# Optimization experiments

Hardware: AMD Instinct MI355X
Metric: run time of the kernel (lower is better)

## Reference

```python
import jax, jax.numpy as jnp
import numpy as np

B, IMG_ROWS, TSTEPS = 64, 32, 128
HID, CIN = 64, 512  # ncde hidden, ncde input dim = 32 * (IMG_ROWS//2)


def _linear(x, w, b):
    return x @ w.T + b


def _conv(x, w, b, pad):
    y = jax.lax.conv_general_dilated(x, w, (1, 1), [(pad, pad), (pad, pad)],
                                     dimension_numbers=('NCHW', 'OIHW', 'NCHW'))
    return y + b[None, :, None, None]


def _maxpool2(x):
    return jax.lax.reduce_window(x, -jnp.inf, jax.lax.max, (1, 1, 2, 2), (1, 1, 2, 2), 'VALID')


def _natural_cubic_coeffs(x):
    # x: [B, L, C], uniform knots t=0..L-1 (h=1). Natural cubic spline.
    L = x.shape[1]
    n = L - 2
    A = 4.0 * jnp.eye(n, dtype=x.dtype) + jnp.eye(n, k=1, dtype=x.dtype) + jnp.eye(n, k=-1, dtype=x.dtype)
    rhs = 6.0 * (x[:, 2:] - 2.0 * x[:, 1:-1] + x[:, :-2])  # [B, n, C]
    Mi = jnp.linalg.solve(A, rhs.transpose(1, 0, 2).reshape(n, -1))
    Mi = Mi.reshape(n, x.shape[0], x.shape[2]).transpose(1, 0, 2)
    M = jnp.pad(Mi, ((0, 0), (1, 1), (0, 0)))  # natural BCs: M0 = M_{L-1} = 0
    a = x[:, :-1]
    b = (x[:, 1:] - x[:, :-1]) - (2.0 * M[:, :-1] + M[:, 1:]) / 6.0
    c = M[:, :-1] / 2.0
    d = (M[:, 1:] - M[:, :-1]) / 6.0
    return a, b, c, d  # each [B, L-1, C]


def _forward(x, conv1_w, conv1_b, conv2_w, conv2_b, att_fc1_w, att_fc1_b,
             att_fc2_w, att_fc2_b, initial_w, initial_b, f1_w, f1_b,
             f2_w, f2_b, out_w, out_b):
    h = jax.nn.relu(_conv(x, conv1_w, conv1_b, pad=2))
    h = jax.nn.relu(_conv(h, conv2_w, conv2_b, pad=1))
    h = _maxpool2(h)  # [B,32,16,T/2]  (dropout is identity in eval)
    att = h.mean(axis=(2, 3))  # AdaptiveAvgPool2d(1)
    att = jax.nn.sigmoid(_linear(jax.nn.relu(_linear(att, att_fc1_w, att_fc1_b)), att_fc2_w, att_fc2_b))
    h = h * att[:, :, None, None]
    h = jnp.transpose(h, (0, 3, 1, 2))
    seq = h.reshape(h.shape[0], h.shape[1], -1)  # [B, L, 512]
    L = seq.shape[1]
    _, sb, sc, sd = _natural_cubic_coeffs(seq)

    z0 = _linear(seq[:, 0], initial_w, initial_b)  # spline.evaluate(t0) == seq[:,0]

    def cdefunc(z):
        u = jax.nn.relu(_linear(z, f1_w, f1_b))
        u = jnp.tanh(_linear(u, f2_w, f2_b))
        return u.reshape(z.shape[0], HID, CIN)

    def dXdt(t):
        seg = jnp.clip(jnp.floor(t).astype(jnp.int32), 0, L - 2)
        fr = t - seg.astype(t.dtype)
        return sb[:, seg] + 2.0 * sc[:, seg] * fr + 3.0 * sd[:, seg] * fr * fr

    def vf(t, z):
        return jnp.einsum('bhc,bc->bh', cdefunc(z), dXdt(t))

    dt = jnp.float32(0.5)
    nsteps = 2 * (L - 1)

    @jax.checkpoint
    def step(z, t):
        k1 = vf(t, z)
        k2 = vf(t + dt / 2, z + dt / 2 * k1)
        k3 = vf(t + dt / 2, z + dt / 2 * k2)
        k4 = vf(t + dt, z + dt * k3)
        return z + dt / 6.0 * (k1 + 2 * k2 + 2 * k3 + k4), None

    ts = jnp.arange(nsteps, dtype=jnp.float32) * dt
    zT, _ = jax.lax.scan(step, z0, ts)
    return _linear(zT, out_w, out_b)


def setup_inputs() -> dict:
    key = jax.random.key(0)
    ks = jax.random.split(key, 10)
    s = lambda k, shape, sc=0.05: (jax.random.normal(k, shape, jnp.float32) * sc)
    z = lambda n: jnp.zeros((n,), jnp.float32)
    return {
        'x': jax.random.normal(ks[0], (B, 1, IMG_ROWS, TSTEPS), jnp.float32),
        'conv1_w': s(ks[1], (32, 1, 5, 5)), 'conv1_b': z(32),
        'conv2_w': s(ks[2], (32, 32, 3, 3)), 'conv2_b': z(32),
        'att_fc1_w': s(ks[3], (4, 32)), 'att_fc1_b': z(4),
        'att_fc2_w': s(ks[4], (32, 4)), 'att_fc2_b': z(32),
        'initial_w': s(ks[5], (HID, CIN)), 'initial_b': z(HID),
        'f1_w': s(ks[6], (128, HID)), 'f1_b': z(128),
        'f2_w': s(ks[7], (CIN * HID, 128)), 'f2_b': z(CIN * HID),
        'out_w': s(ks[8], (2, HID)), 'out_b': z(2),
    }


def reference(x, conv1_w, conv1_b, conv2_w, conv2_b, att_fc1_w, att_fc1_b,
              att_fc2_w, att_fc2_b, initial_w, initial_b, f1_w, f1_b,
              f2_w, f2_b, out_w, out_b):
    return _forward(x, conv1_w, conv1_b, conv2_w, conv2_b, att_fc1_w, att_fc1_b,
                    att_fc2_w, att_fc2_b, initial_w, initial_b, f1_w, f1_b,
                    f2_w, f2_b, out_w, out_b)
```

## Files before the change

### kernel.cpp

```cpp
#include <hip/hip_runtime.h>
#include <hip/hip_bf16.h>
#include <stdint.h>

#define NSTEP 126
#define NEVAL 504
#define POISON 0xAAAAAAAAu

typedef __bf16 v8bf __attribute__((ext_vector_type(8)));
typedef float  v4f  __attribute__((ext_vector_type(4)));

__device__ __forceinline__ unsigned short f2bf(float x) {
  union { float f; uint32_t u; } v; v.f = x;
  uint32_t u = v.u;
  uint32_t r = (u + 0x7FFFu + ((u >> 16) & 1u)) >> 16;
  return (unsigned short)r;
}
__device__ __forceinline__ float bf2f(unsigned short b) {
  union { uint32_t u; float f; } v; v.u = ((uint32_t)b) << 16;
  return v.f;
}
__device__ __forceinline__ uint32_t cvt_pk_bf16(float lo, float hi) {
  uint32_t r;
  asm("v_cvt_pk_bf16_f32 %0, %1, %2" : "=v"(r) : "v"(lo), "v"(hi));
  return r;
}

__global__ void k_detect(const uint32_t* __restrict__ xw, int* flag) {
  __shared__ int cnt;
  if (threadIdx.x == 0) cnt = 0;
  __syncthreads();
  uint32_t w = xw[threadIdx.x];
  int e = (int)((w >> 7) & 0xFF);
  int good = ((e >= 100) && (e <= 144)) || ((w & 0xFFFFu) == 0u);
  atomicAdd(&cnt, good);
  __syncthreads();
  if (threadIdx.x == 0) *flag = (cnt >= 192) ? 1 : 0;
}

#define NCVT 15
struct CvtArgs {
  const void* src[NCVT];
  int dstoff[NCVT];
  int len[NCVT];
  int kind[NCVT];
  int total;
};
__global__ void k_convert(CvtArgs a, float* __restrict__ ws, const int* __restrict__ flag) {
  int f = *flag;
  for (int i = blockIdx.x*256 + threadIdx.x; i < a.total; i += gridDim.x*256) {
    int t = 0; int rem = i;
    while (rem >= a.len[t]) { rem -= a.len[t]; t++; }
    float v = f ? bf2f(((const unsigned short*)a.src[t])[rem])
                : ((const float*)a.src[t])[rem];
    int d;
    if (a.kind[t] == 1) { int h = rem >> 9, c = rem & 511; d = a.dstoff[t] + c*64 + h; }
    else if (a.kind[t] == 2) {
      int co = rem / 288, r2 = rem % 288;
      int ci = r2 / 9, tt = r2 % 9;
      d = a.dstoff[t] + (co >> 4)*4608 + (ci*16 + (co & 15))*9 + tt;
    }
    else d = a.dstoff[t] + rem;
    ws[d] = v;
  }
}

__global__ void k_wbf16(const void* __restrict__ w2src, const void* __restrict__ w1src,
                        unsigned short* __restrict__ w2bf, unsigned short* __restrict__ w1bf,
                        const int* __restrict__ flag) {
  int f = *flag;
  const long N2 = 4194304, N1 = 8192;
  for (long i = (long)blockIdx.x*256 + threadIdx.x; i < N2 + N1; i += (long)gridDim.x*256) {
    if (i < N2) w2bf[i] = f ? ((const unsigned short*)w2src)[i] : f2bf(((const float*)w2src)[i]);
    else { long j = i - N2; w1bf[j] = f ? ((const unsigned short*)w1src)[j] : f2bf(((const float*)w1src)[j]); }
  }
}

__global__ void k_conv1(const float* __restrict__ xf, const float* __restrict__ w,
                        const float* __restrict__ bias, float* __restrict__ h1) {
  int x = threadIdx.x;
  int y = blockIdx.x;
  int b = blockIdx.y;
  const float* xin = xf + (long)b*4096;
  float in[25];
  #pragma unroll
  for (int ky = 0; ky < 5; ky++) {
    int yy = y + ky - 2;
    #pragma unroll
    for (int kx = 0; kx < 5; kx++) {
      int xx = x + kx - 2;
      in[ky*5+kx] = (yy >= 0 && yy < 32 && xx >= 0 && xx < 128) ? xin[yy*128 + xx] : 0.f;
    }
  }
  for (int co = 0; co < 32; co++) {
    float acc = bias[co];
    #pragma unroll
    for (int t = 0; t < 25; t++) acc += in[t] * w[co*25 + t];
    h1[(((long)b*32 + co)*32 + y)*128 + x] = fmaxf(acc, 0.f);
  }
}

#define LD2 132
__global__ __launch_bounds__(256) void k_conv2(const float* __restrict__ h1, const float* __restrict__ w,
                                               const float* __restrict__ bias, float* __restrict__ h2) {
  __shared__ float s[32][3][LD2];
  int y = blockIdx.x, b = blockIdx.y;
  int tid = threadIdx.x;
  for (int i = tid; i < 32*3*LD2; i += 256) {
    int ci = i / (3*LD2);
    int r  = (i / LD2) % 3;
    int xx = i % LD2;
    int yy = y + r - 1, sx = xx - 1;
    float v = 0.f;
    if (yy >= 0 && yy < 32 && sx >= 0 && sx < 128) v = h1[(((long)b*32+ci)*32+yy)*128+sx];
    s[ci][r][xx] = v;
  }
  __syncthreads();
  int x = tid & 127;
  int half = __builtin_amdgcn_readfirstlane(tid >> 7);
  const float* wb = w + half*4608;
  float acc[16];
  #pragma unroll
  for (int i = 0; i < 16; i++) acc[i] = bias[half*16 + i];
  #pragma unroll 2
  for (int ci = 0; ci < 32; ci++) {
    float xv[9];
    #pragma unroll
    for (int r = 0; r < 3; r++)
      #pragma unroll
      for (int k = 0; k < 3; k++) xv[r*3+k] = s[ci][r][x + k];
    #pragma unroll
    for (int co = 0; co < 16; co++) {
      const float* wr = wb + (ci*16 + co)*9;
      #pragma unroll
      for (int t = 0; t < 9; t++) acc[co] += xv[t] * wr[t];
    }
  }
  #pragma unroll
  for (int co = 0; co < 16; co++)
    h2[(((long)b*32 + half*16 + co)*32 + y)*128 + x] = fmaxf(acc[co], 0.f);
}

__global__ void k_pool(const float* __restrict__ h2, float* __restrict__ pooled, float* __restrict__ attm) {
  int bc = blockIdx.x;
  const float* src = h2 + (long)bc*4096;
  float* dst = pooled + (long)bc*1024;
  float sum = 0.f;
  for (int i = threadIdx.x; i < 1024; i += 256) {
    int py = i >> 6, px = i & 63;
    const float* p = src + py*256 + px*2;
    float m = fmaxf(fmaxf(p[0], p[1]), fmaxf(p[128], p[129]));
    dst[i] = m;
    sum += m;
  }
  __shared__ float red[256];
  red[threadIdx.x] = sum;
  __syncthreads();
  for (int s2 = 128; s2 > 0; s2 >>= 1) {
    if (threadIdx.x < s2) red[threadIdx.x] += red[threadIdx.x + s2];
    __syncthreads();
  }
  if (threadIdx.x == 0) attm[bc] = red[0] * (1.f/1024.f);
}

__global__ void k_att(const float* __restrict__ attm, const float* __restrict__ w1, const float* __restrict__ b1,
                      const float* __restrict__ w2, const float* __restrict__ b2, float* __restrict__ atts) {
  int b = threadIdx.x;
  if (b < 64) {
    float hb[4];
    #pragma unroll
    for (int j = 0; j < 4; j++) {
      float s = b1[j];
      for (int i = 0; i < 32; i++) s += attm[b*32+i]*w1[j*32+i];
      hb[j] = fmaxf(s, 0.f);
    }
    for (int o = 0; o < 32; o++) {
      float s = b2[o];
      #pragma unroll
      for (int j = 0; j < 4; j++) s += hb[j]*w2[o*4+j];
      atts[b*32+o] = 1.f/(1.f + __expf(-s));
    }
  }
}

__global__ void k_seq(const float* __restrict__ pooled, const float* __restrict__ atts, float* __restrict__ seq) {
  for (int idx = blockIdx.x*256 + threadIdx.x; idx < 64*64*512; idx += gridDim.x*256) {
    int b = idx >> 15;
    int t = (idx >> 9) & 63;
    int fch = idx & 511;
    int c = fch >> 4, hh = fch & 15;
    seq[idx] = pooled[(((long)b*32 + c)*16 + hh)*64 + t] * atts[b*32 + c];
  }
}

__global__ __launch_bounds__(256, 1) void k_spline(const float* __restrict__ seq,
                                                   float* __restrict__ dxt) {
  int id = blockIdx.x*256 + threadIdx.x;
  int b = id >> 9, f = id & 511;
  const float* xp = seq + (long)b*32768 + f;
  float xv[64];
  #pragma unroll
  for (int t = 0; t < 64; t++) xv[t] = xp[t*512];
  float cp[62], dp[62];
  float pc = 0.f, pd = 0.f;
  #pragma unroll
  for (int i = 0; i < 62; i++) {
    float rhs = 6.f*(xv[i+2] - 2.f*xv[i+1] + xv[i]);
    float inv = 1.f/(4.f - pc);
    pc = inv;
    pd = (rhs - pd)*inv;
    cp[i] = pc; dp[i] = pd;
  }
  #pragma unroll
  for (int i = 60; i >= 0; i--) dp[i] = dp[i] - cp[i]*dp[i+1];
  const float i6 = 1.f/6.f;
  float* op = dxt + (long)b*512 + f;
  #pragma unroll
  for (int t = 0; t < 63; t++) {
    float M0 = (t == 0)  ? 0.f : dp[t-1];
    float M1 = (t == 62) ? 0.f : dp[t];
    float sb = (xv[t+1] - xv[t]) - (2.f*M0 + M1)*i6;
    float sc = 0.5f*M0;
    float sd = (M1 - M0)*i6;
    float* o = op + (long)(4*t)*32768;
    o[0]      = sb;
    o[32768]  = sb + 0.5f*sc + 0.1875f*sd;
    o[65536]  = sb + sc + 0.75f*sd;
    o[98304]  = sb + 1.5f*sc + 1.6875f*sd;
    if (t == 62) o[131072] = sb + 2.f*sc + 3.f*sd;
  }
}

__global__ void k_z0(const float* __restrict__ seq, const float* __restrict__ iwT,
                     const float* __restrict__ ib, float* __restrict__ z0) {
  __shared__ float s0[512];
  int b = blockIdx.x, h = threadIdx.x;
  for (int c = h; c < 512; c += 64) s0[c] = seq[(long)b*32768 + c];
  __syncthreads();
  float acc = ib[h];
  for (int c = 0; c < 512; c++) acc += s0[c]*iwT[c*64 + h];
  z0[b*64 + h] = acc;
}

__global__ __launch_bounds__(512, 2) void k_ode(
    const float* __restrict__ z0buf,
    const unsigned short* __restrict__ w2bf,
    const unsigned short* __restrict__ w1bf,
    const float* __restrict__ f1bias,
    const float* __restrict__ f2bias,
    const float* __restrict__ dxt,
    const float* __restrict__ outw,
    const float* __restrict__ outb,
    uint32_t* kpart,
    void* dout,
    const int* __restrict__ flag)
{
  __shared__ __align__(16) unsigned short zs[16*72];
  __shared__ __align__(16) unsigned short ub[16*136];
  __shared__ __align__(16) float dxs[16*524 + 9600];
  __shared__ __align__(16) uint32_t klds[1024];
  __shared__ float kred[128];

  int tid = threadIdx.x;
  int bl  = blockIdx.x;
  int hb  = bl >> 2;
  int bq  = bl & 3;
  int B0  = bq*16;
  int lane = tid & 63, wv = tid >> 6;
  int q = lane >> 4, ln = lane & 15;

  v8bf w2f[4][4];
  #pragma unroll
  for (int jt = 0; jt < 4; jt++)
    #pragma unroll
    for (int ks = 0; ks < 4; ks++) {
      long row = (long)hb*512 + wv*64 + jt*16 + ln;
      w2f[jt][ks] = *(const v8bf*)(w2bf + row*128 + ks*32 + q*8);
    }
  v8bf w1f[2];
  #pragma unroll
  for (int ks = 0; ks < 2; ks++)
    w1f[ks] = *(const v8bf*)(w1bf + (wv*16 + ln)*64 + ks*32 + q*8);
  float fb2[4][4];
  #pragma unroll
  for (int jt = 0; jt < 4; jt++)
    #pragma unroll
    for (int r = 0; r < 4; r++)
      fb2[jt][r] = f2bias[(long)hb*512 + wv*64 + jt*16 + q*4 + r];
  float fb1[4];
  #pragma unroll
  for (int r = 0; r < 4; r++)
    fb1[r] = f1bias[wv*16 + q*4 + r];

  int zbL = tid & 15;
  int hg  = tid >> 4;
  int h0  = hg*2;
  float z[2], zacc[2];
  #pragma unroll
  for (int i = 0; i < 2; i++) { z[i] = z0buf[(B0+zbL)*64 + h0 + i]; zacc[i] = 0.f; }

  const float dt6 = 0.5f/6.f;
  int e = 0;
  for (int step = 0; step < NSTEP; step++) {
    #pragma unroll 1
    for (int stage = 0; stage < 4; stage++, e++) {
      bool do_dx = (stage == 1) || (stage == 3) || (e == 0);
      int m = 2*step + ((stage + 1) >> 1);
      float4 dxr[4];
      if (do_dx) {
        #pragma unroll
        for (int i = 0; i < 4; i++) {
          int fi = i*512 + tid;
          int bb = fi >> 7, c4 = fi & 127;
          dxr[i] = *(const float4*)(dxt + (long)m*32768 + (B0+bb)*512 + c4*4);
        }
      }
      if (e > 0) {
        const uint32_t* kp = kpart + ((long)(e-1)*4 + bq)*1024;
        if (tid >= 64 && tid < 320) {
          int pt = tid - 64;
          const uint32_t* pp = kp + pt*4;
          uint32_t v0 = __hip_atomic_load(pp+0, __ATOMIC_RELAXED, __HIP_MEMORY_SCOPE_AGENT);
          uint32_t v1 = __hip_atomic_load(pp+1, __ATOMIC_RELAXED, __HIP_MEMORY_SCOPE_AGENT);
          uint32_t v2 = __hip_atomic_load(pp+2, __ATOMIC_RELAXED, __HIP_MEMORY_SCOPE_AGENT);
          uint32_t v3 = __hip_atomic_load(pp+3, __ATOMIC_RELAXED, __HIP_MEMORY_SCOPE_AGENT);
          while (v0 == POISON) { __builtin_amdgcn_s_sleep(1);
            v0 = __hip_atomic_load(pp+0, __ATOMIC_RELAXED, __HIP_MEMORY_SCOPE_AGENT); }
          while (v1 == POISON) { __builtin_amdgcn_s_sleep(1);
            v1 = __hip_atomic_load(pp+1, __ATOMIC_RELAXED, __HIP_MEMORY_SCOPE_AGENT); }
          while (v2 == POISON) { __builtin_amdgcn_s_sleep(1);
            v2 = __hip_atomic_load(pp+2, __ATOMIC_RELAXED, __HIP_MEMORY_SCOPE_AGENT); }
          while (v3 == POISON) { __builtin_amdgcn_s_sleep(1);
            v3 = __hip_atomic_load(pp+3, __ATOMIC_RELAXED, __HIP_MEMORY_SCOPE_AGENT); }
          uint4 w4; w4.x = v0; w4.y = v1; w4.z = v2; w4.w = v3;
          *(uint4*)(klds + pt*4) = w4;
        }
        __syncthreads();
        if (do_dx) {
          #pragma unroll
          for (int i = 0; i < 4; i++) {
            int fi = i*512 + tid;
            int bb = fi >> 7, c4 = fi & 127;
            *(float4*)(dxs + bb*524 + c4*4) = dxr[i];
          }
        }
        float kv0 = __uint_as_float(klds[h0*16 + zbL]);
        float kv1 = __uint_as_float(klds[(h0+1)*16 + zbL]);
        if (stage == 0) {
          z[0] += dt6*(zacc[0] + kv0);
          z[1] += dt6*(zacc[1] + kv1);
          zacc[0] = 0.f; zacc[1] = 0.f;
          *(uint32_t*)(zs + zbL*72 + h0) = cvt_pk_bf16(z[0], z[1]);
        } else {
          float wk = (stage == 1) ? 1.f : 2.f;
          float aa = (stage == 3) ? 0.5f : 0.25f;
          zacc[0] += wk*kv0;
          zacc[1] += wk*kv1;
          *(uint32_t*)(zs + zbL*72 + h0) = cvt_pk_bf16(z[0] + aa*kv0, z[1] + aa*kv1);
        }
      } else {
        *(uint32_t*)(zs + zbL*72 + h0) = cvt_pk_bf16(z[0], z[1]);
        if (do_dx) {
          #pragma unroll
          for (int i = 0; i < 4; i++) {
            int fi = i*512 + tid;
            int bb = fi >> 7, c4 = fi & 127;
            *(float4*)(dxs + bb*524 + c4*4) = dxr[i];
          }
        }
      }
      __syncthreads();
      v8bf zf[2];
      #pragma unroll
      for (int ks = 0; ks < 2; ks++)
        zf[ks] = *(const v8bf*)(zs + ln*72 + ks*32 + q*8);
      {
        v4f ua = (v4f){fb1[0], fb1[1], fb1[2], fb1[3]};
        #pragma unroll
        for (int ks = 0; ks < 2; ks++)
          ua = __builtin_amdgcn_mfma_f32_16x16x32_bf16(w1f[ks], zf[ks], ua, 0, 0, 0);
        uint2 upk;
        upk.x = cvt_pk_bf16(fmaxf(ua[0], 0.f), fmaxf(ua[1], 0.f));
        upk.y = cvt_pk_bf16(fmaxf(ua[2], 0.f), fmaxf(ua[3], 0.f));
        *(uint2*)(ub + ln*136 + wv*16 + q*4) = upk;
      }
      __syncthreads();
      v8bf uf[4];
      #pragma unroll
      for (int ks = 0; ks < 4; ks++)
        uf[ks] = *(const v8bf*)(ub + ln*136 + ks*32 + q*8);
      float ksum = 0.f;
      #pragma unroll
      for (int jt = 0; jt < 4; jt++) {
        v4f acc = (v4f){fb2[jt][0], fb2[jt][1], fb2[jt][2], fb2[jt][3]};
        #pragma unroll
        for (int ks = 0; ks < 4; ks++)
          acc = __builtin_amdgcn_mfma_f32_16x16x32_bf16(w2f[jt][ks], uf[ks], acc, 0, 0, 0);
        v4f dx4 = *(const v4f*)(dxs + ln*524 + wv*64 + jt*16 + q*4);
        #pragma unroll
        for (int r = 0; r < 4; r++) {
          float xv2 = acc[r];
          float ex = __expf(2.f*xv2);
          float th = 1.f - 2.f*__builtin_amdgcn_rcpf(ex + 1.f);
          ksum += th*dx4[r];
        }
      }
      ksum += __shfl_xor(ksum, 16, 64);
      ksum += __shfl_xor(ksum, 32, 64);
      if (lane < 16)
        kred[ln*8 + wv] = ksum;
      __syncthreads();
      if (tid < 16) {
        const float* kr = kred + tid*8;
        float v = ((((((kr[0]+kr[1])+kr[2])+kr[3])+kr[4])+kr[5])+kr[6])+kr[7];
        uint32_t uv = __float_as_uint(v);
        if (uv == POISON) uv ^= 1u;
        __hip_atomic_store(kpart + (((long)e*4 + bq)*64 + hb)*16 + tid, uv,
                           __ATOMIC_RELAXED, __HIP_MEMORY_SCOPE_AGENT);
      }
    }
  }
  if (hb == 0) {
    const uint32_t* kp = kpart + ((long)(NEVAL-1)*4 + bq)*1024;
    if (tid >= 64 && tid < 128) {
      const uint32_t* pp = kp + (tid - 64)*16;
      while (__hip_atomic_load(pp, __ATOMIC_RELAXED, __HIP_MEMORY_SCOPE_AGENT) == POISON)
        __builtin_amdgcn_s_sleep(1);
    }
    __syncthreads();
    {
      #pragma unroll
      for (int i = 0; i < 2; i++) {
        const uint32_t* p = kp + (h0+i)*16 + zbL;
        uint32_t v = __hip_atomic_load(p, __ATOMIC_RELAXED, __HIP_MEMORY_SCOPE_AGENT);
        while (v == POISON) {
          __builtin_amdgcn_s_sleep(1);
          v = __hip_atomic_load(p, __ATOMIC_RELAXED, __HIP_MEMORY_SCOPE_AGENT);
        }
        z[i] += dt6*(zacc[i] + __uint_as_float(v));
      }
    }
    float o0 = z[0]*outw[h0] + z[1]*outw[h0+1];
    float o1 = z[0]*outw[64+h0] + z[1]*outw[64+h0+1];
    __syncthreads();
    dxs[hg*32 + zbL*2 + 0] = o0;
    dxs[hg*32 + zbL*2 + 1] = o1;
    __syncthreads();
    if (tid < 32) {
      int bloc = tid >> 1, comp = tid & 1;
      float s = outb[comp];
      #pragma unroll
      for (int g = 0; g < 32; g++) s += dxs[g*32 + bloc*2 + comp];
      int b = B0 + bloc;
      if (*flag) ((unsigned short*)dout)[b*2 + comp] = f2bf(s);
      else       ((float*)dout)[b*2 + comp] = s;
    }
  }
}

extern "C" void kernel_launch(void* const* d_in, const int* in_sizes, int n_in,
                              void* d_out, int out_size, void* d_ws, size_t ws_size,
                              hipStream_t stream) {
  (void)in_sizes; (void)n_in; (void)out_size; (void)ws_size;
  float* ws = (float*)d_ws;
  size_t o = 0;
  auto alloc = [&](size_t n) { size_t r = o; o += (n + 63) & ~(size_t)63; return r; };
  size_t o_flag = alloc(64);
  size_t o_xf   = alloc(262144);
  size_t o_c1w  = alloc(800);
  size_t o_c1b  = alloc(32);
  size_t o_c2w  = alloc(9216);
  size_t o_c2b  = alloc(32);
  size_t o_a1w  = alloc(128);
  size_t o_a1b  = alloc(4);
  size_t o_a2w  = alloc(128);
  size_t o_a2b  = alloc(32);
  size_t o_iwT  = alloc(32768);
  size_t o_ib   = alloc(64);
  size_t o_f1b  = alloc(128);
  size_t o_f2b  = alloc(32768);
  size_t o_ow   = alloc(128);
  size_t o_ob   = alloc(2);
  size_t o_z0   = alloc(4096);
  size_t o_attm = alloc(2048);
  size_t o_atts = alloc(2048);
  size_t o_w1bf = alloc(4096);
  size_t o_w2bf = alloc(2097152);
  size_t o_h1   = alloc(8388608);
  size_t o_h2   = alloc(8388608);
  size_t o_kpart= alloc(4128768);
  size_t o_pool = o_h1;
  size_t o_seq  = o_h1 + 2097152;
  size_t o_dxt  = o_h2;

  int* flag = (int*)(ws + o_flag);

  hipLaunchKernelGGL(k_detect, dim3(1), dim3(256), 0, stream, (const uint32_t*)d_in[0], flag);

  CvtArgs ca;
  const int  si[NCVT]  = {0,1,2,3,4,5,6,7,8,9,10,12,14,15,16};
  const size_t dofs[NCVT] = {o_xf,o_c1w,o_c1b,o_c2w,o_c2b,o_a1w,o_a1b,o_a2w,o_a2b,o_iwT,o_ib,o_f1b,o_f2b,o_ow,o_ob};
  const int  ln[NCVT]  = {262144,800,32,9216,32,128,4,128,32,32768,64,128,32768,128,2};
  int tot = 0;
  for (int i = 0; i < NCVT; i++) {
    ca.src[i] = d_in[si[i]];
    ca.dstoff[i] = (int)dofs[i];
    ca.len[i] = ln[i];
    ca.kind[i] = (si[i] == 9) ? 1 : ((si[i] == 3) ? 2 : 0);
    tot += ln[i];
  }
  ca.total = tot;
  hipLaunchKernelGGL(k_convert, dim3(512), dim3(256), 0, stream, ca, ws, flag);
  hipLaunchKernelGGL(k_wbf16, dim3(2048), dim3(256), 0, stream, d_in[13], d_in[11],
                     (unsigned short*)(ws + o_w2bf), (unsigned short*)(ws + o_w1bf), flag);
  hipLaunchKernelGGL(k_conv1, dim3(32,64), dim3(128), 0, stream, ws+o_xf, ws+o_c1w, ws+o_c1b, ws+o_h1);
  hipLaunchKernelGGL(k_conv2, dim3(32,64), dim3(256), 0, stream, ws+o_h1, ws+o_c2w, ws+o_c2b, ws+o_h2);
  hipLaunchKernelGGL(k_pool, dim3(2048), dim3(256), 0, stream, ws+o_h2, ws+o_pool, ws+o_attm);
  hipLaunchKernelGGL(k_att, dim3(1), dim3(64), 0, stream, ws+o_attm, ws+o_a1w, ws+o_a1b, ws+o_a2w, ws+o_a2b, ws+o_atts);
  hipLaunchKernelGGL(k_seq, dim3(2048), dim3(256), 0, stream, ws+o_pool, ws+o_atts, ws+o_seq);
  hipLaunchKernelGGL(k_spline, dim3(128), dim3(256), 0, stream, ws+o_seq, ws+o_dxt);
  hipLaunchKernelGGL(k_z0, dim3(64), dim3(64), 0, stream, ws+o_seq, ws+o_iwT, ws+o_ib, ws+o_z0);

  hipLaunchKernelGGL(k_ode, dim3(256), dim3(512), 0, stream,
                     ws + o_z0,
                     (const unsigned short*)(ws + o_w2bf),
                     (const unsigned short*)(ws + o_w1bf),
                     ws + o_f1b, ws + o_f2b,
                     ws + o_dxt, ws + o_ow, ws + o_ob,
                     (uint32_t*)(ws + o_kpart),
                     d_out, (const int*)flag);
}
```

Measured before the change: 1.704 ms.

## Interleave two batch quarters per ODE block to hide cross-block spin latency

Each ODE block now processes two independent 16-sample batch groups in alternation, with half as many blocks launched. While one group waits for its cross-block k-partial exchange, the other group computes, and the poll of the other group's partials is issued early. The dx spline slice is prefetched into registers one stage ahead, and the barriers become raw s_barrier calls that wait only on LDS counters. This trades per-block parallelism and higher register and LDS use for hiding the serial inter-block dependency latency.

```diff
diff --git a/kernel.cpp b/kernel.cpp
--- a/kernel.cpp
+++ b/kernel.cpp
@@ -24,6 +24,8 @@
   asm("v_cvt_pk_bf16_f32 %0, %1, %2" : "=v"(r) : "v"(lo), "v"(hi));
   return r;
 }
+
+#define BARL() asm volatile("s_waitcnt lgkmcnt(0)\n\ts_barrier" ::: "memory")
 
 __global__ void k_detect(const uint32_t* __restrict__ xw, int* flag) {
   __shared__ int cnt;
@@ -241,6 +243,7 @@
   z0[b*64 + h] = acc;
 }
 
+#define DXSZ (16*524 + 1024)
 __global__ __launch_bounds__(512, 2) void k_ode(
     const float* __restrict__ z0buf,
     const unsigned short* __restrict__ w2bf,
@@ -256,15 +259,16 @@
 {
   __shared__ __align__(16) unsigned short zs[16*72];
   __shared__ __align__(16) unsigned short ub[16*136];
-  __shared__ __align__(16) float dxs[16*524 + 9600];
-  __shared__ __align__(16) uint32_t klds[1024];
+  __shared__ __align__(16) float dxsA[DXSZ];
+  __shared__ __align__(16) float dxsB[DXSZ];
   __shared__ float kred[128];
 
   int tid = threadIdx.x;
   int bl  = blockIdx.x;
-  int hb  = bl >> 2;
-  int bq  = bl & 3;
-  int B0  = bq*16;
+  int hb  = bl >> 1;
+  int bqp = bl & 1;
+  int cqA = bqp,     B0A = bqp*16;
+  int cqB = bqp + 2, B0B = bqp*16 + 32;
   int lane = tid & 63, wv = tid >> 6;
   int q = lane >> 4, ln = lane & 15;
 
@@ -294,140 +298,154 @@
   int zbL = tid & 15;
   int hg  = tid >> 4;
   int h0  = hg*2;
-  float z[2], zacc[2];
-  #pragma unroll
-  for (int i = 0; i < 2; i++) { z[i] = z0buf[(B0+zbL)*64 + h0 + i]; zacc[i] = 0.f; }
+  float zA[2], zaA[2], zB[2], zaB[2];
+  #pragma unroll
+  for (int i = 0; i < 2; i++) {
+    zA[i] = z0buf[(B0A+zbL)*64 + h0 + i]; zaA[i] = 0.f;
+    zB[i] = z0buf[(B0B+zbL)*64 + h0 + i]; zaB[i] = 0.f;
+  }
+
+  uint32_t kvA[2], kvB[2];
+  float4 dxrA[4], dxrB[4];
+  #pragma unroll
+  for (int i = 0; i < 4; i++) {
+    int fi = i*512 + tid;
+    int bb = fi >> 7, c4 = fi & 127;
+    dxrA[i] = *(const float4*)(dxt + (B0A+bb)*512 + c4*4);
+    dxrB[i] = *(const float4*)(dxt + (B0B+bb)*512 + c4*4);
+  }
 
   const float dt6 = 0.5f/6.f;
-  int e = 0;
-  for (int step = 0; step < NSTEP; step++) {
-    #pragma unroll 1
-    for (int stage = 0; stage < 4; stage++, e++) {
-      bool do_dx = (stage == 1) || (stage == 3) || (e == 0);
-      int m = 2*step + ((stage + 1) >> 1);
-      float4 dxr[4];
-      if (do_dx) {
-        #pragma unroll
-        for (int i = 0; i < 4; i++) {
-          int fi = i*512 + tid;
-          int bb = fi >> 7, c4 = fi & 127;
-          dxr[i] = *(const float4*)(dxt + (long)m*32768 + (B0+bb)*512 + c4*4);
+
+  auto STAGE = [&](int e, int cq, int B0,
+                   float (&z)[2], float (&za)[2], uint32_t (&kv)[2],
+                   float4 (&dxr)[4], float (&dxs)[DXSZ],
+                   int eIs, int cqIs, uint32_t (&kvIs)[2], bool isValid) {
+    int st = e & 3;
+    bool dodx = (e & 1) || (e == 0);
+    if (isValid) {
+      const uint32_t* kp2 = kpart + ((long)eIs*4 + cqIs)*1024;
+      kvIs[0] = __hip_atomic_load(kp2 + (h0+0)*16 + zbL, __ATOMIC_RELAXED, __HIP_MEMORY_SCOPE_AGENT);
+      kvIs[1] = __hip_atomic_load(kp2 + (h0+1)*16 + zbL, __ATOMIC_RELAXED, __HIP_MEMORY_SCOPE_AGENT);
+    }
+    if (e > 0) {
+      const uint32_t* kp = kpart + ((long)(e-1)*4 + cq)*1024;
+      float kvf[2];
+      #pragma unroll
+      for (int i = 0; i < 2; i++) {
+        uint32_t v = kv[i];
+        const uint32_t* p = kp + (h0+i)*16 + zbL;
+        while (v == POISON) {
+          __builtin_amdgcn_s_sleep(1);
+          v = __hip_atomic_load(p, __ATOMIC_RELAXED, __HIP_MEMORY_SCOPE_AGENT);
         }
-      }
-      if (e > 0) {
-        const uint32_t* kp = kpart + ((long)(e-1)*4 + bq)*1024;
-        if (tid >= 64 && tid < 320) {
-          int pt = tid - 64;
-          const uint32_t* pp = kp + pt*4;
-          uint32_t v0 = __hip_atomic_load(pp+0, __ATOMIC_RELAXED, __HIP_MEMORY_SCOPE_AGENT);
-          uint32_t v1 = __hip_atomic_load(pp+1, __ATOMIC_RELAXED, __HIP_MEMORY_SCOPE_AGENT);
-          uint32_t v2 = __hip_atomic_load(pp+2, __ATOMIC_RELAXED, __HIP_MEMORY_SCOPE_AGENT);
-          uint32_t v3 = __hip_atomic_load(pp+3, __ATOMIC_RELAXED, __HIP_MEMORY_SCOPE_AGENT);
-          while (v0 == POISON) { __builtin_amdgcn_s_sleep(1);
-            v0 = __hip_atomic_load(pp+0, __ATOMIC_RELAXED, __HIP_MEMORY_SCOPE_AGENT); }
-          while (v1 == POISON) { __builtin_amdgcn_s_sleep(1);
-            v1 = __hip_atomic_load(pp+1, __ATOMIC_RELAXED, __HIP_MEMORY_SCOPE_AGENT); }
-          while (v2 == POISON) { __builtin_amdgcn_s_sleep(1);
-            v2 = __hip_atomic_load(pp+2, __ATOMIC_RELAXED, __HIP_MEMORY_SCOPE_AGENT); }
-          while (v3 == POISON) { __builtin_amdgcn_s_sleep(1);
-            v3 = __hip_atomic_load(pp+3, __ATOMIC_RELAXED, __HIP_MEMORY_SCOPE_AGENT); }
-          uint4 w4; w4.x = v0; w4.y = v1; w4.z = v2; w4.w = v3;
-          *(uint4*)(klds + pt*4) = w4;
+        kvf[i] = __uint_as_float(v);
+      }
+      if (st == 0) {
+        z[0] += dt6*(za[0] + kvf[0]);
+        z[1] += dt6*(za[1] + kvf[1]);
+        za[0] = 0.f; za[1] = 0.f;
+        *(uint32_t*)(zs + zbL*72 + h0) = cvt_pk_bf16(z[0], z[1]);
+      } else {
+        float wk = (st == 1) ? 1.f : 2.f;
+        float aa = (st == 3) ? 0.5f : 0.25f;
+        za[0] += wk*kvf[0];
+        za[1] += wk*kvf[1];
+        *(uint32_t*)(zs + zbL*72 + h0) = cvt_pk_bf16(z[0] + aa*kvf[0], z[1] + aa*kvf[1]);
+      }
+    } else {
+      *(uint32_t*)(zs + zbL*72 + h0) = cvt_pk_bf16(z[0], z[1]);
+    }
+    if (dodx) {
+      #pragma unroll
+      for (int i = 0; i < 4; i++) {
+        int fi = i*512 + tid;
+        int bb = fi >> 7, c4 = fi & 127;
+        *(float4*)(dxs + bb*524 + c4*4) = dxr[i];
+      }
+    }
+    if (!(e & 1)) {
+      int mn = ((e+1) >> 2)*2 + ((((e+1) & 3) + 1) >> 1);
+      #pragma unroll
+      for (int i = 0; i < 4; i++) {
+        int fi = i*512 + tid;
+        int bb = fi >> 7, c4 = fi & 127;
+        dxr[i] = *(const float4*)(dxt + (long)mn*32768 + (B0+bb)*512 + c4*4);
+      }
+    }
+    BARL();
+    v8bf zf[2];
+    #pragma unroll
+    for (int ks = 0; ks < 2; ks++)
+      zf[ks] = *(const v8bf*)(zs + ln*72 + ks*32 + q*8);
+    {
+      v4f ua = (v4f){fb1[0], fb1[1], fb1[2], fb1[3]};
+      #pragma unroll
+      for (int ks = 0; ks < 2; ks++)
+        ua = __builtin_amdgcn_mfma_f32_16x16x32_bf16(w1f[ks], zf[ks], ua, 0, 0, 0);
+      uint2 upk;
+      upk.x = cvt_pk_bf16(fmaxf(ua[0], 0.f), fmaxf(ua[1], 0.f));
+      upk.y = cvt_pk_bf16(fmaxf(ua[2], 0.f), fmaxf(ua[3], 0.f));
+      *(uint2*)(ub + ln*136 + wv*16 + q*4) = upk;
+    }
+    BARL();
+    v8bf uf[4];
+    #pragma unroll
+    for (int ks = 0; ks < 4; ks++)
+      uf[ks] = *(const v8bf*)(ub + ln*136 + ks*32 + q*8);
+    float ksum = 0.f;
+    #pragma unroll
+    for (int jt = 0; jt < 4; jt++) {
+      v4f acc = (v4f){fb2[jt][0], fb2[jt][1], fb2[jt][2], fb2[jt][3]};
+      #pragma unroll
+      for (int ks = 0; ks < 4; ks++)
+        acc = __builtin_amdgcn_mfma_f32_16x16x32_bf16(w2f[jt][ks], uf[ks], acc, 0, 0, 0);
+      v4f dx4 = *(const v4f*)(dxs + ln*524 + wv*64 + jt*16 + q*4);
+      #pragma unroll
+      for (int r = 0; r < 4; r++) {
+        float xv2 = acc[r];
+        float ex = __expf(2.f*xv2);
+        float th = 1.f - 2.f*__builtin_amdgcn_rcpf(ex + 1.f);
+        ksum += th*dx4[r];
+      }
+    }
+    ksum += __shfl_xor(ksum, 16, 64);
+    ksum += __shfl_xor(ksum, 32, 64);
+    if (lane < 16)
+      kred[ln*8 + wv] = ksum;
+    BARL();
+    if (tid < 16) {
+      const float* kr = kred + tid*8;
+      float v = ((((((kr[0]+kr[1])+kr[2])+kr[3])+kr[4])+kr[5])+kr[6])+kr[7];
+      uint32_t uv = __float_as_uint(v);
+      if (uv == POISON) uv ^= 1u;
+      __hip_atomic_store(kpart + (((long)e*4 + cq)*64 + hb)*16 + tid, uv,
+                         __ATOMIC_RELAXED, __HIP_MEMORY_SCOPE_AGENT);
+    }
+  };
+
+  #pragma unroll 1
+  for (int e = 0; e < NEVAL; e++) {
+    STAGE(e, cqA, B0A, zA, zaA, kvA, dxrA, dxsA, e-1, cqB, kvB, (e >= 1));
+    STAGE(e, cqB, B0B, zB, zaB, kvB, dxrB, dxsB, e,   cqA, kvA, true);
+  }
+
+  if (hb == 0) {
+    {
+      const uint32_t* kp = kpart + ((long)(NEVAL-1)*4 + cqA)*1024;
+      #pragma unroll
+      for (int i = 0; i < 2; i++) {
+        uint32_t v = kvA[i];
+        const uint32_t* p = kp + (h0+i)*16 + zbL;
+        while (v == POISON) {
+          __builtin_amdgcn_s_sleep(1);
+          v = __hip_atomic_load(p, __ATOMIC_RELAXED, __HIP_MEMORY_SCOPE_AGENT);
         }
-        __syncthreads();
-        if (do_dx) {
-          #pragma unroll
-          for (int i = 0; i < 4; i++) {
-            int fi = i*512 + tid;
-            int bb = fi >> 7, c4 = fi & 127;
-            *(float4*)(dxs + bb*524 + c4*4) = dxr[i];
-          }
-        }
-        float kv0 = __uint_as_float(klds[h0*16 + zbL]);
-        float kv1 = __uint_as_float(klds[(h0+1)*16 + zbL]);
-        if (stage == 0) {
-          z[0] += dt6*(zacc[0] + kv0);
-          z[1] += dt6*(zacc[1] + kv1);
-          zacc[0] = 0.f; zacc[1] = 0.f;
-          *(uint32_t*)(zs + zbL*72 + h0) = cvt_pk_bf16(z[0], z[1]);
-        } else {
-          float wk = (stage == 1) ? 1.f : 2.f;
-          float aa = (stage == 3) ? 0.5f : 0.25f;
-          zacc[0] += wk*kv0;
-          zacc[1] += wk*kv1;
-          *(uint32_t*)(zs + zbL*72 + h0) = cvt_pk_bf16(z[0] + aa*kv0, z[1] + aa*kv1);
-        }
-      } else {
-        *(uint32_t*)(zs + zbL*72 + h0) = cvt_pk_bf16(z[0], z[1]);
-        if (do_dx) {
-          #pragma unroll
-          for (int i = 0; i < 4; i++) {
-            int fi = i*512 + tid;
-            int bb = fi >> 7, c4 = fi & 127;
-            *(float4*)(dxs + bb*524 + c4*4) = dxr[i];
-          }
-        }
-      }
-      __syncthreads();
-      v8bf zf[2];
-      #pragma unroll
-      for (int ks = 0; ks < 2; ks++)
-        zf[ks] = *(const v8bf*)(zs + ln*72 + ks*32 + q*8);
-      {
-        v4f ua = (v4f){fb1[0], fb1[1], fb1[2], fb1[3]};
-        #pragma unroll
-        for (int ks = 0; ks < 2; ks++)
-          ua = __builtin_amdgcn_mfma_f32_16x16x32_bf16(w1f[ks], zf[ks], ua, 0, 0, 0);
-        uint2 upk;
-        upk.x = cvt_pk_bf16(fmaxf(ua[0], 0.f), fmaxf(ua[1], 0.f));
-        upk.y = cvt_pk_bf16(fmaxf(ua[2], 0.f), fmaxf(ua[3], 0.f));
-        *(uint2*)(ub + ln*136 + wv*16 + q*4) = upk;
-      }
-      __syncthreads();
-      v8bf uf[4];
-      #pragma unroll
-      for (int ks = 0; ks < 4; ks++)
-        uf[ks] = *(const v8bf*)(ub + ln*136 + ks*32 + q*8);
-      float ksum = 0.f;
-      #pragma unroll
-      for (int jt = 0; jt < 4; jt++) {
-        v4f acc = (v4f){fb2[jt][0], fb2[jt][1], fb2[jt][2], fb2[jt][3]};
-        #pragma unroll
-        for (int ks = 0; ks < 4; ks++)
-          acc = __builtin_amdgcn_mfma_f32_16x16x32_bf16(w2f[jt][ks], uf[ks], acc, 0, 0, 0);
-        v4f dx4 = *(const v4f*)(dxs + ln*524 + wv*64 + jt*16 + q*4);
-        #pragma unroll
-        for (int r = 0; r < 4; r++) {
-          float xv2 = acc[r];
-          float ex = __expf(2.f*xv2);
-          float th = 1.f - 2.f*__builtin_amdgcn_rcpf(ex + 1.f);
-          ksum += th*dx4[r];
-        }
-      }
-      ksum += __shfl_xor(ksum, 16, 64);
-      ksum += __shfl_xor(ksum, 32, 64);
-      if (lane < 16)
-        kred[ln*8 + wv] = ksum;
-      __syncthreads();
-      if (tid < 16) {
-        const float* kr = kred + tid*8;
-        float v = ((((((kr[0]+kr[1])+kr[2])+kr[3])+kr[4])+kr[5])+kr[6])+kr[7];
-        uint32_t uv = __float_as_uint(v);
-        if (uv == POISON) uv ^= 1u;
-        __hip_atomic_store(kpart + (((long)e*4 + bq)*64 + hb)*16 + tid, uv,
-                           __ATOMIC_RELAXED, __HIP_MEMORY_SCOPE_AGENT);
-      }
-    }
-  }
-  if (hb == 0) {
-    const uint32_t* kp = kpart + ((long)(NEVAL-1)*4 + bq)*1024;
-    if (tid >= 64 && tid < 128) {
-      const uint32_t* pp = kp + (tid - 64)*16;
-      while (__hip_atomic_load(pp, __ATOMIC_RELAXED, __HIP_MEMORY_SCOPE_AGENT) == POISON)
-        __builtin_amdgcn_s_sleep(1);
-    }
-    __syncthreads();
+        zA[i] += dt6*(zaA[i] + __uint_as_float(v));
+      }
+    }
     {
+      const uint32_t* kp = kpart + ((long)(NEVAL-1)*4 + cqB)*1024;
       #pragma unroll
       for (int i = 0; i < 2; i++) {
         const uint32_t* p = kp + (h0+i)*16 + zbL;
@@ -436,23 +454,43 @@
           __builtin_amdgcn_s_sleep(1);
           v = __hip_atomic_load(p, __ATOMIC_RELAXED, __HIP_MEMORY_SCOPE_AGENT);
         }
-        z[i] += dt6*(zacc[i] + __uint_as_float(v));
-      }
-    }
-    float o0 = z[0]*outw[h0] + z[1]*outw[h0+1];
-    float o1 = z[0]*outw[64+h0] + z[1]*outw[64+h0+1];
-    __syncthreads();
-    dxs[hg*32 + zbL*2 + 0] = o0;
-    dxs[hg*32 + zbL*2 + 1] = o1;
-    __syncthreads();
-    if (tid < 32) {
-      int bloc = tid >> 1, comp = tid & 1;
-      float s = outb[comp];
-      #pragma unroll
-      for (int g = 0; g < 32; g++) s += dxs[g*32 + bloc*2 + comp];
-      int b = B0 + bloc;
-      if (*flag) ((unsigned short*)dout)[b*2 + comp] = f2bf(s);
-      else       ((float*)dout)[b*2 + comp] = s;
+        zB[i] += dt6*(zaB[i] + __uint_as_float(v));
+      }
+    }
+    int fl = *flag;
+    {
+      float o0 = zA[0]*outw[h0] + zA[1]*outw[h0+1];
+      float o1 = zA[0]*outw[64+h0] + zA[1]*outw[64+h0+1];
+      BARL();
+      dxsA[hg*32 + zbL*2 + 0] = o0;
+      dxsA[hg*32 + zbL*2 + 1] = o1;
+      BARL();
+      if (tid < 32) {
+        int bloc = tid >> 1, comp = tid & 1;
+        float s = outb[comp];
+        #pragma unroll
+        for (int g = 0; g < 32; g++) s += dxsA[g*32 + bloc*2 + comp];
+        int b = B0A + bloc;
+        if (fl) ((unsigned short*)dout)[b*2 + comp] = f2bf(s);
+        else    ((float*)dout)[b*2 + comp] = s;
+      }
+      BARL();
+    }
+    {
+      float o0 = zB[0]*outw[h0] + zB[1]*outw[h0+1];
+      float o1 = zB[0]*outw[64+h0] + zB[1]*outw[64+h0+1];
+      dxsA[hg*32 + zbL*2 + 0] = o0;
+      dxsA[hg*32 + zbL*2 + 1] = o1;
+      BARL();
+      if (tid < 32) {
+        int bloc = tid >> 1, comp = tid & 1;
+        float s = outb[comp];
+        #pragma unroll
+        for (int g = 0; g < 32; g++) s += dxsA[g*32 + bloc*2 + comp];
+        int b = B0B + bloc;
+        if (fl) ((unsigned short*)dout)[b*2 + comp] = f2bf(s);
+        else    ((float*)dout)[b*2 + comp] = s;
+      }
     }
   }
 }
@@ -520,7 +558,7 @@
   hipLaunchKernelGGL(k_spline, dim3(128), dim3(256), 0, stream, ws+o_seq, ws+o_dxt);
   hipLaunchKernelGGL(k_z0, dim3(64), dim3(64), 0, stream, ws+o_seq, ws+o_iwT, ws+o_ib, ws+o_z0);
 
-  hipLaunchKernelGGL(k_ode, dim3(256), dim3(512), 0, stream,
+  hipLaunchKernelGGL(k_ode, dim3(128), dim3(512), 0, stream,
                      ws + o_z0,
                      (const unsigned short*)(ws + o_w2bf),
                      (const unsigned short*)(ws + o_w1bf),
```

Result: slower. 2.745 ms (+61.0%).
